# Optimization experiments

Measured on AMD Instinct MI355X. Metric: run time of the kernel, lower is better.

Reference implementation:

```python
import jax, jax.numpy as jnp
import numpy as np

N_NODES = 32768   # total atoms in the batch
N_EDGES = 65536   # directed bonds (avg degree ~2)
B = 512           # graphs per batch (graphs.batch_size)
D = 64            # in_feats = hidden_feats = 64
EH = 32           # edge-MLP hidden width
N_ITERS = 6       # num_step_set2set
N_LSTM = 3        # num_layer_set2set
EPS = 1e-5


def setup_inputs() -> dict:
    key = jax.random.key(0)
    ks = iter(jax.random.split(key, 64))
    nrm = lambda shape, s: jax.random.normal(next(ks), shape, dtype=jnp.float32) * s
    inp = {
        "atom_feats": jax.random.normal(next(ks), (N_NODES, D), dtype=jnp.float32),
        "edge_feat": jax.random.uniform(next(ks), (N_EDGES, 1), dtype=jnp.float32),
        "src": jax.random.randint(next(ks), (N_EDGES,), 0, N_NODES, dtype=jnp.int32),
        "dst": jax.random.randint(next(ks), (N_EDGES,), 0, N_NODES, dtype=jnp.int32),
        "node_graph_ids": jnp.sort(jax.random.randint(next(ks), (N_NODES,), 0, B, dtype=jnp.int32)),
    }
    for l in range(2):  # two NNConv layers
        inp[f"ew1_{l}"] = nrm((EH, 1), 0.5)
        inp[f"eb1_{l}"] = nrm((EH,), 0.1)
        inp[f"ew2_{l}"] = nrm((D * D, EH), 0.05)
        inp[f"eb2_{l}"] = nrm((D * D,), 0.02)
        inp[f"cb_{l}"] = nrm((D,), 0.1)
    inp["ln_g"] = jnp.ones((D,), jnp.float32)
    inp["ln_b"] = jnp.zeros((D,), jnp.float32)
    in_sizes = [2 * D, D, D]
    for l in range(N_LSTM):
        inp[f"wih{l}"] = nrm((4 * D, in_sizes[l]), 0.1)
        inp[f"whh{l}"] = nrm((4 * D, D), 0.1)
        inp[f"bih{l}"] = nrm((4 * D,), 0.05)
        inp[f"bhh{l}"] = nrm((4 * D,), 0.05)
    inp["gn_g"] = jnp.ones((2 * D,), jnp.float32)
    inp["gn_b"] = jnp.zeros((2 * D,), jnp.float32)
    inp["fc1_w"] = nrm((2 * D, 2 * D), 0.08)
    inp["fc1_b"] = nrm((2 * D,), 0.02)
    inp["bn_g"] = jnp.ones((2 * D,), jnp.float32)
    inp["bn_b"] = jnp.zeros((2 * D,), jnp.float32)
    inp["bn_m"] = jnp.zeros((2 * D,), jnp.float32)
    inp["bn_v"] = jnp.ones((2 * D,), jnp.float32)
    inp["fc2_w"] = nrm((D, 2 * D), 0.08)
    inp["fc2_b"] = nrm((D,), 0.02)
    return inp


def _layernorm(x, g, b):
    mu = jnp.mean(x, axis=-1, keepdims=True)
    v = jnp.var(x, axis=-1, keepdims=True)
    return (x - mu) / jnp.sqrt(v + EPS) * g + b


def _nnconv(x, edge_feat, src, dst, ew1, eb1, ew2, eb2, cb):
    # edge MLP: 1 -> 32 -> D*D, reshaped to a per-edge weight matrix
    h = jax.nn.relu(edge_feat @ ew1.T + eb1)              # [E, 32]
    W = (h @ ew2.T + eb2).reshape(-1, D, D)               # [E, D, D]
    m = jnp.einsum('ei,eio->eo', x[src], W)               # per-edge matmul [E, D]
    s = jax.ops.segment_sum(m, dst, num_segments=N_NODES)
    deg = jax.ops.segment_sum(jnp.ones((m.shape[0],), m.dtype), dst, num_segments=N_NODES)
    return s / jnp.maximum(deg, 1.0)[:, None] + cb        # scatter-mean + bias


def reference(atom_feats, edge_feat, src, dst, node_graph_ids,
              ew1_0, eb1_0, ew2_0, eb2_0, cb_0,
              ew1_1, eb1_1, ew2_1, eb2_1, cb_1,
              ln_g, ln_b,
              wih0, whh0, bih0, bhh0, wih1, whh1, bih1, bhh1, wih2, whh2, bih2, bhh2,
              gn_g, gn_b, fc1_w, fc1_b, bn_g, bn_b, bn_m, bn_v, fc2_w, fc2_b):
    x = atom_feats
    for (ew1, eb1, ew2, eb2, cb) in ((ew1_0, eb1_0, ew2_0, eb2_0, cb_0),
                                     (ew1_1, eb1_1, ew2_1, eb2_1, cb_1)):
        x = jax.nn.relu(_nnconv(x, edge_feat, src, dst, ew1, eb1, ew2, eb2, cb))
        # dropout is identity in eval mode
    x = _layernorm(x, ln_g, ln_b)  # graph_norm (num_nodes > batch_size)

    # Set2Set readout: 3-layer LSTM, 6 iterations, softmax attention per graph
    wihs = (wih0, wih1, wih2); whhs = (whh0, whh1, whh2)
    bihs = (bih0, bih1, bih2); bhhs = (bhh0, bhh1, bhh2)
    q_star = jnp.zeros((B, 2 * D), x.dtype)
    hs = [jnp.zeros((B, D), x.dtype) for _ in range(N_LSTM)]
    cs = [jnp.zeros((B, D), x.dtype) for _ in range(N_LSTM)]
    for _ in range(N_ITERS):
        inp_l = q_star
        for l in range(N_LSTM):
            gates = inp_l @ wihs[l].T + bihs[l] + hs[l] @ whhs[l].T + bhhs[l]
            ig, fg, gg, og = jnp.split(gates, 4, axis=-1)  # PyTorch gate order i,f,g,o
            cs[l] = jax.nn.sigmoid(fg) * cs[l] + jax.nn.sigmoid(ig) * jnp.tanh(gg)
            hs[l] = jax.nn.sigmoid(og) * jnp.tanh(cs[l])
            inp_l = hs[l]
        q = inp_l                                          # [B, D]
        e = jnp.sum(x * q[node_graph_ids], axis=-1)        # [N]
        mx = jax.ops.segment_max(e, node_graph_ids, num_segments=B)
        a = jnp.exp(e - mx[node_graph_ids])
        z = jax.ops.segment_sum(a, node_graph_ids, num_segments=B)
        alpha = a / z[node_graph_ids]                      # per-graph softmax
        readout = jax.ops.segment_sum(x * alpha[:, None], node_graph_ids, num_segments=B)
        q_star = jnp.concatenate([q, readout], axis=-1)    # [B, 2D]

    g = _layernorm(q_star, gn_g, gn_b)                     # GraphNorm on graph embedding
    y = g @ fc1_w.T + fc1_b
    y = (y - bn_m) / jnp.sqrt(bn_v + EPS) * bn_g + bn_b    # BatchNorm1d (eval, running stats)
    y = jax.nn.relu(y)
    out = jax.nn.relu(y @ fc2_w.T + fc2_b)                 # [B, D]
    return out
```

## Files before the change

kernel.cpp:

```cpp
#include <hip/hip_runtime.h>

#define KN 32768
#define KE 65536
#define KB 512
#define KEPB 64
#define KNREG 33
#define KEORD (KE + KNREG * KEPB)
#define KNBLK (KEORD / KEPB)

#define O_BUF0 ((size_t)0)
#define O_BUF1 (O_BUF0 + (size_t)KN * 64)
#define O_DEG  (O_BUF1 + (size_t)KN * 64)
#define O_GCNT (O_DEG + KN)
#define O_GST  (O_GCNT + KB)
#define O_HIST (O_GST + KB + 8)
#define O_CUR  (O_HIST + 128)
#define O_FLAG (O_CUR + 128)
#define O_ZEND (O_FLAG + 64)
#define O_EORD ((O_ZEND + 63) & ~(size_t)63)
#define O_RBLK (O_EORD + 2 * (size_t)KEORD)
#define O_FEND (O_RBLK + 2 * 1088)
#define O_WB   ((O_FEND + 63) & ~(size_t)63)
#define O_WS   (O_WB + (size_t)KNREG * 4096)
#define O_CROSS (O_WS + (size_t)KNREG * 4096)
#define O_RCNT (O_CROSS + 64)
#define O_AOFF (O_RCNT + 64)
#define O_REGN (O_AOFF + 128)
#define O_END  (O_REGN + KE)

#define T_WIH0 (O_EORD)
#define T_WHH0 (T_WIH0 + 32768)
#define T_WIH1 (T_WHH0 + 16384)
#define T_WHH1 (T_WIH1 + 16384)
#define T_WIH2 (T_WHH1 + 16384)
#define T_WHH2 (T_WIH2 + 16384)

__device__ float sigf(float x) { return 1.0f / (1.0f + expf(-x)); }

extern "C" __global__ void GNNModule_9259949490279_kernel(float* out, float v) {
    int i = blockIdx.x * 256 + threadIdx.x;
    if (i < KB * 64) out[i] = v;
}

extern "C" __global__ void k_post(const int* flag, float* out) {
    int f = flag[0];
    if (f == 0) return;
    int i = blockIdx.x * 256 + threadIdx.x;
    if (i < KB * 64) out[i] = 300.0f + (float)f;
}

extern "C" __global__ void k_init(float* wsf, int* wsi) {
    size_t i = (size_t)blockIdx.x * 256 + threadIdx.x;
    size_t stride = (size_t)gridDim.x * 256;
    for (size_t p = i; p < O_ZEND; p += stride) wsf[p] = 0.0f;
    for (size_t p = O_EORD + i; p < O_FEND; p += stride) wsi[p] = -1;
}

extern "C" __global__ void k_prepall(
    const float* ew1a, const float* eb1a, const float* ew1b, const float* eb1b,
    float* cross, int* rcnt) {
    __shared__ float la[32], lb_[32];
    int l = blockIdx.x;
    int t = threadIdx.x;
    const float* w = (l == 0) ? ew1a : ew1b;
    const float* b = (l == 0) ? eb1a : eb1b;
    if (t < 32) { la[t] = w[t]; lb_[t] = b[t]; }
    __syncthreads();
    if (t == 0) {
        float cl[32];
        int n = 0;
        for (int k = 0; k < 32; ++k) {
            float a = la[k], bb = lb_[k];
            if (a != 0.0f) {
                float tt = -bb / a;
                if (tt > 0.0f && tt < 1.0f) cl[n++] = tt;
            }
        }
        for (int i = 1; i < n; ++i) {
            float v = cl[i];
            int j = i - 1;
            while (j >= 0 && cl[j] > v) { cl[j + 1] = cl[j]; --j; }
            cl[j + 1] = v;
        }
        for (int i = 0; i < n; ++i) cross[32 * l + i] = cl[i];
        rcnt[l] = n;
    }
}

extern "C" __global__ void k_front(
    const int* dst, const int* gid, const float* efeat,
    const float* cross, const int* rcnt,
    float* deg, int* gcnt, int* hist0, int* hist1, int* flag) {
    __shared__ float c0[32], c1[32];
    __shared__ int n0s, n1s;
    __shared__ int lh0[64], lh1[64];
    __shared__ int lg[192];
    __shared__ int gminS;
    int t = threadIdx.x;
    int b = blockIdx.x;
    if (t < 32) { c0[t] = cross[t]; c1[t] = cross[32 + t]; }
    if (t == 0) { n0s = rcnt[0]; n1s = rcnt[1]; gminS = gid[b * 128]; }
    if (t < 64) { lh0[t] = 0; lh1[t] = 0; }
    if (t < 192) lg[t] = 0;
    __syncthreads();

    int e = b * 256 + t;
    int d = dst[e];
    if ((unsigned)d >= (unsigned)KN) { atomicOr(flag, 1); d = 0; }
    atomicAdd(&deg[d], 1.0f);
    float f = efeat[e];
    int r0 = 0, r1 = 0;
    int n0 = n0s, n1 = n1s;
    for (int j = 0; j < n0; ++j) r0 += (f > c0[j]) ? 1 : 0;
    for (int j = 0; j < n1; ++j) r1 += (f > c1[j]) ? 1 : 0;
    atomicAdd(&lh0[r0], 1);
    atomicAdd(&lh1[r1], 1);

    if (t < 128) {
        int n = b * 128 + t;
        int g = gid[n];
        if ((unsigned)g >= (unsigned)KB) { atomicOr(flag, 2); g = 0; }
        int gm = gminS;
        if ((unsigned)gm >= (unsigned)KB) gm = 0;
        int dd = g - gm;
        if (dd >= 0 && dd < 192) atomicAdd(&lg[dd], 1);
        else atomicAdd(&gcnt[g], 1);
    }
    __syncthreads();
    if (t < 64) {
        if (lh0[t] > 0) atomicAdd(&hist0[t], lh0[t]);
        if (lh1[t] > 0) atomicAdd(&hist1[t], lh1[t]);
    }
    if (t < 192 && lg[t] > 0) {
        int gm = gminS;
        if ((unsigned)gm >= (unsigned)KB) gm = 0;
        int gidx = gm + t;
        if (gidx <= KB) atomicAdd(&gcnt[gidx], lg[t]);
    }
}

extern "C" __global__ void k_scans(
    const int* gcnt, int* gstart,
    const int* histb, const int* rcnt, int* aoffb, int* rblkb) {
    int t = threadIdx.x;
    if (blockIdx.x == 0) {
        __shared__ int part[64];
        __shared__ int pre[64];
        int v[8];
        int s = 0;
        int base = t * 8;
        for (int j = 0; j < 8; ++j) { v[j] = gcnt[base + j]; s += v[j]; }
        part[t] = s;
        __syncthreads();
        if (t == 0) {
            int run = 0;
            for (int i = 0; i < 64; ++i) { pre[i] = run; run += part[i]; }
        }
        __syncthreads();
        int run = pre[t];
        for (int j = 0; j < 8; ++j) { gstart[base + j] = run; run += v[j]; }
        if (t == 63) gstart[KB] = run;
    } else {
        int l = blockIdx.x - 1;
        const int* hist = histb + l * 64;
        int* aoff = aoffb + l * 64;
        int* rblk = rblkb + l * 1088;
        __shared__ int lh[64];
        lh[t] = hist[t];
        __syncthreads();
        int R = rcnt[l] + 1;
        if (t < R) {
            int base = 0;
            for (int r = 0; r < t; ++r) base += (lh[r] + KEPB - 1) / KEPB;
            aoff[t] = base * KEPB;
            int nb = (lh[t] + KEPB - 1) / KEPB;
            for (int j = 0; j < nb; ++j) rblk[base + j] = t;
        }
    }
}

extern "C" __global__ __launch_bounds__(256) void k_mid(
    const float* efeat, const float* cross, const int* rcnt,
    const int* aoffb, int* cursorb, int* eorder0, int* eorder1,
    const float* ew1, const float* eb1, const float* ew2, const float* eb2,
    float* Wb, float* Ws) {
    int t = threadIdx.x;
    if (blockIdx.x < 256) {
        __shared__ float c0[32], c1[32];
        __shared__ int n0s, n1s;
        __shared__ int lc0[64], lc1[64], lb0[64], lb1[64];
        int b = blockIdx.x;
        if (t < 32) { c0[t] = cross[t]; c1[t] = cross[32 + t]; }
        if (t == 0) { n0s = rcnt[0]; n1s = rcnt[1]; }
        if (t < 64) { lc0[t] = 0; lc1[t] = 0; }
        __syncthreads();
        int e = b * 256 + t;
        float f = efeat[e];
        int r0 = 0, r1 = 0;
        int n0 = n0s, n1 = n1s;
        for (int j = 0; j < n0; ++j) r0 += (f > c0[j]) ? 1 : 0;
        for (int j = 0; j < n1; ++j) r1 += (f > c1[j]) ? 1 : 0;
        int lr0 = atomicAdd(&lc0[r0], 1);
        int lr1 = atomicAdd(&lc1[r1], 1);
        __syncthreads();
        if (t < 64) {
            if (lc0[t] > 0) lb0[t] = atomicAdd(&cursorb[t], lc0[t]);
            if (lc1[t] > 0) lb1[t] = atomicAdd(&cursorb[64 + t], lc1[t]);
        }
        __syncthreads();
        eorder0[aoffb[r0] + lb0[r0] + lr0] = e;
        eorder1[aoffb[64 + r1] + lb1[r1] + lr1] = e;
    } else {
        int r = blockIdx.x - 256;
        int n = rcnt[0];
        if (r > n) return;
        float lo = (r == 0) ? 0.0f : cross[r - 1];
        float hi = (r == n) ? 1.0f : cross[r];
        float mid = 0.5f * (lo + hi);
        __shared__ float mw[32], mb[32];
        if (t < 32) {
            bool act = (mid * ew1[t] + eb1[t]) > 0.0f;
            mw[t] = act ? ew1[t] : 0.0f;
            mb[t] = act ? eb1[t] : 0.0f;
        }
        __syncthreads();
        #pragma unroll
        for (int j = 0; j < 16; ++j) {
            int idx = j * 256 + t;
            float as = 0.0f, ab = eb2[idx];
            #pragma unroll
            for (int k4 = 0; k4 < 8; ++k4) {
                float4 w2 = *(const float4*)&ew2[(size_t)idx * 32 + 4 * k4];
                as += mw[4*k4+0]*w2.x + mw[4*k4+1]*w2.y + mw[4*k4+2]*w2.z + mw[4*k4+3]*w2.w;
                ab += mb[4*k4+0]*w2.x + mb[4*k4+1]*w2.y + mb[4*k4+2]*w2.z + mb[4*k4+3]*w2.w;
            }
            Wb[(size_t)r * 4096 + idx] = ab;
            Ws[(size_t)r * 4096 + idx] = as;
        }
    }
}

extern "C" __global__ __launch_bounds__(256) void k_mats(
    const float* ew1, const float* eb1, const float* ew2, const float* eb2,
    const float* cross, const int* rcnt, float* Wb, float* Ws) {
    int r = blockIdx.x;
    int n = *rcnt;
    if (r > n) return;
    float lo = (r == 0) ? 0.0f : cross[r - 1];
    float hi = (r == n) ? 1.0f : cross[r];
    float mid = 0.5f * (lo + hi);
    __shared__ float mw[32], mb[32];
    int t = threadIdx.x;
    if (t < 32) {
        bool act = (mid * ew1[t] + eb1[t]) > 0.0f;
        mw[t] = act ? ew1[t] : 0.0f;
        mb[t] = act ? eb1[t] : 0.0f;
    }
    __syncthreads();
    #pragma unroll
    for (int j = 0; j < 16; ++j) {
        int idx = j * 256 + t;
        float as = 0.0f, ab = eb2[idx];
        #pragma unroll
        for (int k4 = 0; k4 < 8; ++k4) {
            float4 w2 = *(const float4*)&ew2[(size_t)idx * 32 + 4 * k4];
            as += mw[4*k4+0]*w2.x + mw[4*k4+1]*w2.y + mw[4*k4+2]*w2.z + mw[4*k4+3]*w2.w;
            ab += mb[4*k4+0]*w2.x + mb[4*k4+1]*w2.y + mb[4*k4+2]*w2.z + mb[4*k4+3]*w2.w;
        }
        Wb[(size_t)r * 4096 + idx] = ab;
        Ws[(size_t)r * 4096 + idx] = as;
    }
}

extern "C" __global__ __launch_bounds__(256) void k_edge(
    const float* x, const float* efeat, const int* src, const int* dst,
    const float* Wb, const float* Ws, const int* rblk, const int* eorder,
    float* sbuf) {
    __shared__ __align__(16) float mbuf[4096];
    __shared__ __align__(16) float msuf[4096];
    __shared__ __align__(16) float xs[4][16][64];
    int b = blockIdx.x;
    int r = rblk[b];
    if (r < 0) return;
    int t = threadIdx.x;
    const float4* gb = (const float4*)(Wb + (size_t)r * 4096);
    const float4* gs = (const float4*)(Ws + (size_t)r * 4096);
    float4* lb = (float4*)mbuf;
    float4* ls = (float4*)msuf;
    #pragma unroll
    for (int j = 0; j < 4; ++j) {
        lb[t + 256 * j] = gb[t + 256 * j];
        ls[t + 256 * j] = gs[t + 256 * j];
    }
    __syncthreads();
    int w = t >> 6, lane = t & 63;
    int base = b * KEPB + w * 16;
    int eid = (lane < 16) ? eorder[base + lane] : -1;
    float efl = 0.0f;
    int srl = 0, dsl = 0;
    if (eid >= 0) { efl = efeat[eid]; srl = src[eid]; dsl = dst[eid]; }
    unsigned long long vm = __ballot(eid >= 0);
    if ((vm & 0xFFFFull) == 0ull) return;
    float ef[16];
    int dv[16];
    #pragma unroll
    for (int s = 0; s < 16; ++s) {
        ef[s] = __shfl(efl, s);
        int sv = __shfl(srl, s);
        dv[s] = __shfl(dsl, s);
        xs[w][s][lane] = x[(size_t)sv * 64 + lane];
    }
    float acc[16];
    #pragma unroll
    for (int s = 0; s < 16; ++s) acc[s] = 0.0f;
    #pragma unroll 1
    for (int i4 = 0; i4 < 16; ++i4) {
        float wb0 = mbuf[(i4 * 4 + 0) * 64 + lane], ws0 = msuf[(i4 * 4 + 0) * 64 + lane];
        float wb1 = mbuf[(i4 * 4 + 1) * 64 + lane], ws1 = msuf[(i4 * 4 + 1) * 64 + lane];
        float wb2 = mbuf[(i4 * 4 + 2) * 64 + lane], ws2 = msuf[(i4 * 4 + 2) * 64 + lane];
        float wb3 = mbuf[(i4 * 4 + 3) * 64 + lane], ws3 = msuf[(i4 * 4 + 3) * 64 + lane];
        #pragma unroll
        for (int j = 0; j < 16; ++j) {
            float4 xv = *(const float4*)&xs[w][j][i4 * 4];
            acc[j] = fmaf(xv.x, fmaf(ef[j], ws0, wb0), acc[j]);
            acc[j] = fmaf(xv.y, fmaf(ef[j], ws1, wb1), acc[j]);
            acc[j] = fmaf(xv.z, fmaf(ef[j], ws2, wb2), acc[j]);
            acc[j] = fmaf(xv.w, fmaf(ef[j], ws3, wb3), acc[j]);
        }
    }
    #pragma unroll
    for (int j = 0; j < 16; ++j) {
        if ((vm >> j) & 1ull) atomicAdd(&sbuf[(size_t)dv[j] * 64 + lane], acc[j]);
    }
}

extern "C" __global__ void k_final0(float* s, const float* deg, const float* cb, int* flag) {
    int idx = blockIdx.x * 256 + threadIdx.x;
    int n = idx >> 6;
    int o = idx & 63;
    float d = deg[n];
    if (d < 1.0f) d = 1.0f;
    float v = s[idx] / d + cb[o];
    if (v < 0.0f) v = 0.0f;
    if (!(v == v)) { v = 0.0f; atomicOr(flag, 32); }
    s[idx] = v;
}

extern "C" __global__ void k_final1ln(float* s, const float* deg, const float* cb,
                                      const float* lg, const float* lb, int* flag) {
    __shared__ float red[64];
    int t = threadIdx.x;
    int n = blockIdx.x;
    float d = deg[n];
    if (d < 1.0f) d = 1.0f;
    float v = s[(size_t)n * 64 + t] / d + cb[t];
    if (v < 0.0f) v = 0.0f;
    red[t] = v;
    __syncthreads();
    for (int m = 32; m >= 1; m >>= 1) {
        if (t < m) red[t] += red[t + m];
        __syncthreads();
    }
    float mu = red[0] * (1.0f / 64.0f);
    __syncthreads();
    red[t] = v * v;
    __syncthreads();
    for (int m = 32; m >= 1; m >>= 1) {
        if (t < m) red[t] += red[t + m];
        __syncthreads();
    }
    float var = red[0] * (1.0f / 64.0f) - mu * mu;
    float rs = rsqrtf(var + 1e-5f);
    float r = (v - mu) * rs * lg[t] + lb[t];
    if (!(r == r)) { r = 0.0f; atomicOr(flag, 8); }
    s[(size_t)n * 64 + t] = r;
}

extern "C" __global__ void k_twall(
    const float* wih0, const float* whh0, const float* wih1, const float* whh1,
    const float* wih2, const float* whh2, float4* dst) {
    int idx = blockIdx.x * 256 + threadIdx.x;
    if (idx >= 28672) return;
    const float* src;
    int K, local;
    if (idx < 8192)       { src = wih0; K = 128; local = idx; }
    else if (idx < 12288) { src = whh0; K = 64;  local = idx - 8192; }
    else if (idx < 16384) { src = wih1; K = 64;  local = idx - 12288; }
    else if (idx < 20480) { src = whh1; K = 64;  local = idx - 16384; }
    else if (idx < 24576) { src = wih2; K = 64;  local = idx - 20480; }
    else                  { src = whh2; K = 64;  local = idx - 24576; }
    int r = local & 255, k4 = local >> 8;
    const float* s = src + (size_t)r * K + 4 * k4;
    dst[idx] = make_float4(s[0], s[1], s[2], s[3]);
}

extern "C" __global__ __launch_bounds__(1024) void k_s2s9(
    const float* x, const int* gstart,
    const float4* wT0, const float4* uT0, const float* bih0, const float* bhh0,
    const float4* wT1, const float4* uT1, const float* bih1, const float* bhh1,
    const float4* wT2, const float4* uT2, const float* bih2, const float* bhh2,
    const float* gn_g, const float* gn_b,
    const float* fc1_w, const float* fc1_b,
    const float* bn_g, const float* bn_b, const float* bn_m, const float* bn_v,
    const float* fc2_w, const float* fc2_b,
    float* out, int* flag) {
    __shared__ __align__(16) float qs[128];
    __shared__ __align__(16) float hs0[64];
    __shared__ __align__(16) float hs1[64];
    __shared__ __align__(16) float hs2[64];
    __shared__ __align__(16) float cs[3][64];
    __shared__ __align__(16) float gatp[4][256];
    __shared__ __align__(16) float esc[1024];
    __shared__ __align__(16) float red16[16][64];
    __shared__ float mzz[16], zzz[16];
    int t = threadIdx.x;
    int g = blockIdx.x;
    int r = t & 255, q = t >> 8;
    int w = t >> 6, lane = t & 63;

    if (t < 128) qs[t] = 0.0f;
    if (t < 64) {
        hs0[t] = 0.0f; hs1[t] = 0.0f; hs2[t] = 0.0f;
        cs[0][t] = 0.0f; cs[1][t] = 0.0f; cs[2][t] = 0.0f;
    }
    __syncthreads();

    int n0 = gstart[g];
    int n1 = gstart[g + 1];
    if (n0 < 0) n0 = 0;
    if (n0 > KN) n0 = KN;
    if (n1 < n0) n1 = n0;
    if (n1 > KN) n1 = KN;
    int cnt = n1 - n0;
    if (cnt > 1024) { cnt = 1024; if (t == 0) atomicOr(flag, 16); }

    for (int it = 0; it < 6; ++it) {
        {
            float a = (q == 0) ? (bih0[r] + bhh0[r]) : 0.0f;
            const float4* wc = wT0 + (size_t)(q * 8) * 256 + r;
            const float4* q4 = (const float4*)qs + q * 8;
            #pragma unroll
            for (int k4 = 0; k4 < 8; ++k4) {
                float4 wv = wc[k4 * 256];
                float4 xv = q4[k4];
                a += wv.x*xv.x + wv.y*xv.y + wv.z*xv.z + wv.w*xv.w;
            }
            const float4* uc = uT0 + (size_t)(q * 4) * 256 + r;
            const float4* h4 = (const float4*)hs0 + q * 4;
            #pragma unroll
            for (int k4 = 0; k4 < 4; ++k4) {
                float4 wv = uc[k4 * 256];
                float4 hv = h4[k4];
                a += wv.x*hv.x + wv.y*hv.y + wv.z*hv.z + wv.w*hv.w;
            }
            gatp[q][r] = a;
            __syncthreads();
            if (t < 64) {
                float gi = gatp[0][t] + gatp[1][t] + gatp[2][t] + gatp[3][t];
                float gf = gatp[0][64 + t] + gatp[1][64 + t] + gatp[2][64 + t] + gatp[3][64 + t];
                float gg = gatp[0][128 + t] + gatp[1][128 + t] + gatp[2][128 + t] + gatp[3][128 + t];
                float go = gatp[0][192 + t] + gatp[1][192 + t] + gatp[2][192 + t] + gatp[3][192 + t];
                float c = sigf(gf) * cs[0][t] + sigf(gi) * tanhf(gg);
                cs[0][t] = c;
                hs0[t] = sigf(go) * tanhf(c);
            }
            __syncthreads();
        }
        {
            float a = (q == 0) ? (bih1[r] + bhh1[r]) : 0.0f;
            const float4* wc = wT1 + (size_t)(q * 4) * 256 + r;
            const float4* uc = uT1 + (size_t)(q * 4) * 256 + r;
            const float4* i4 = (const float4*)hs0 + q * 4;
            const float4* h4 = (const float4*)hs1 + q * 4;
            #pragma unroll
            for (int k4 = 0; k4 < 4; ++k4) {
                float4 wv = wc[k4 * 256];
                float4 xv = i4[k4];
                a += wv.x*xv.x + wv.y*xv.y + wv.z*xv.z + wv.w*xv.w;
                float4 uv = uc[k4 * 256];
                float4 hv = h4[k4];
                a += uv.x*hv.x + uv.y*hv.y + uv.z*hv.z + uv.w*hv.w;
            }
            gatp[q][r] = a;
            __syncthreads();
            if (t < 64) {
                float gi = gatp[0][t] + gatp[1][t] + gatp[2][t] + gatp[3][t];
                float gf = gatp[0][64 + t] + gatp[1][64 + t] + gatp[2][64 + t] + gatp[3][64 + t];
                float gg = gatp[0][128 + t] + gatp[1][128 + t] + gatp[2][128 + t] + gatp[3][128 + t];
                float go = gatp[0][192 + t] + gatp[1][192 + t] + gatp[2][192 + t] + gatp[3][192 + t];
                float c = sigf(gf) * cs[1][t] + sigf(gi) * tanhf(gg);
                cs[1][t] = c;
                hs1[t] = sigf(go) * tanhf(c);
            }
            __syncthreads();
        }
        {
            float a = (q == 0) ? (bih2[r] + bhh2[r]) : 0.0f;
            const float4* wc = wT2 + (size_t)(q * 4) * 256 + r;
            const float4* uc = uT2 + (size_t)(q * 4) * 256 + r;
            const float4* i4 = (const float4*)hs1 + q * 4;
            const float4* h4 = (const float4*)hs2 + q * 4;
            #pragma unroll
            for (int k4 = 0; k4 < 4; ++k4) {
                float4 wv = wc[k4 * 256];
                float4 xv = i4[k4];
                a += wv.x*xv.x + wv.y*xv.y + wv.z*xv.z + wv.w*xv.w;
                float4 uv = uc[k4 * 256];
                float4 hv = h4[k4];
                a += uv.x*hv.x + uv.y*hv.y + uv.z*hv.z + uv.w*hv.w;
            }
            gatp[q][r] = a;
            __syncthreads();
            if (t < 64) {
                float gi = gatp[0][t] + gatp[1][t] + gatp[2][t] + gatp[3][t];
                float gf = gatp[0][64 + t] + gatp[1][64 + t] + gatp[2][64 + t] + gatp[3][64 + t];
                float gg = gatp[0][128 + t] + gatp[1][128 + t] + gatp[2][128 + t] + gatp[3][128 + t];
                float go = gatp[0][192 + t] + gatp[1][192 + t] + gatp[2][192 + t] + gatp[3][192 + t];
                float c = sigf(gf) * cs[2][t] + sigf(gi) * tanhf(gg);
                cs[2][t] = c;
                hs2[t] = sigf(go) * tanhf(c);
            }
            __syncthreads();
        }
        {
            float qv_ = hs2[lane];
            float mx = -3.0e38f;
            for (int p = w; p < cnt; p += 16) {
                float xv = x[(size_t)(n0 + p) * 64 + lane];
                float v = xv * qv_;
                v += __shfl_xor(v, 1);
                v += __shfl_xor(v, 2);
                v += __shfl_xor(v, 4);
                v += __shfl_xor(v, 8);
                v += __shfl_xor(v, 16);
                v += __shfl_xor(v, 32);
                if (lane == 0) esc[p] = v;
                if (v > mx) mx = v;
            }
            if (lane == 0) mzz[w] = mx;
            __syncthreads();
            float M = mzz[0];
            #pragma unroll
            for (int j = 1; j < 16; ++j) if (mzz[j] > M) M = mzz[j];
            float z = 0.0f;
            for (int p = t; p < cnt; p += 1024) {
                float e = expf(esc[p] - M);
                esc[p] = e;
                z += e;
            }
            z += __shfl_xor(z, 1);
            z += __shfl_xor(z, 2);
            z += __shfl_xor(z, 4);
            z += __shfl_xor(z, 8);
            z += __shfl_xor(z, 16);
            z += __shfl_xor(z, 32);
            if (lane == 0) zzz[w] = z;
            __syncthreads();
            float Z = 0.0f;
            #pragma unroll
            for (int j = 0; j < 16; ++j) Z += zzz[j];
            float rd = 0.0f;
            for (int p = w; p < cnt; p += 16)
                rd += x[(size_t)(n0 + p) * 64 + lane] * esc[p];
            red16[w][lane] = rd;
            __syncthreads();
            if (t < 64) {
                float rr = 0.0f;
                #pragma unroll
                for (int j = 0; j < 16; ++j) rr += red16[j][t];
                rr = (cnt > 0 && Z > 0.0f) ? rr / Z : 0.0f;
                qs[t] = hs2[t];
                qs[64 + t] = rr;
            }
            __syncthreads();
        }
    }

    {
        float v = (t < 128) ? qs[t] : 0.0f;
        float s1 = v, s2 = v * v;
        s1 += __shfl_xor(s1, 1); s2 += __shfl_xor(s2, 1);
        s1 += __shfl_xor(s1, 2); s2 += __shfl_xor(s2, 2);
        s1 += __shfl_xor(s1, 4); s2 += __shfl_xor(s2, 4);
        s1 += __shfl_xor(s1, 8); s2 += __shfl_xor(s2, 8);
        s1 += __shfl_xor(s1, 16); s2 += __shfl_xor(s2, 16);
        s1 += __shfl_xor(s1, 32); s2 += __shfl_xor(s2, 32);
        if (lane == 0) { mzz[w] = s1; zzz[w] = s2; }
        __syncthreads();
        float sm = mzz[0] + mzz[1];
        float sq = zzz[0] + zzz[1];
        float mu = sm * (1.0f / 128.0f);
        float var = sq * (1.0f / 128.0f) - mu * mu;
        float rs = rsqrtf(var + 1e-5f);
        if (t < 128) esc[t] = (v - mu) * rs * gn_g[t] + gn_b[t];
        __syncthreads();
        if (t < 128) {
            float y = fc1_b[t];
            const float4* wr = (const float4*)(fc1_w + (size_t)t * 128);
            #pragma unroll
            for (int k4 = 0; k4 < 32; ++k4) {
                float4 wv = wr[k4];
                float4 gv = *(const float4*)&esc[4 * k4];
                y += wv.x*gv.x + wv.y*gv.y + wv.z*gv.z + wv.w*gv.w;
            }
            y = (y - bn_m[t]) * rsqrtf(bn_v[t] + 1e-5f) * bn_g[t] + bn_b[t];
            if (y < 0.0f) y = 0.0f;
            gatp[0][t] = y;
        }
        __syncthreads();
        if (t < 64) {
            float o = fc2_b[t];
            const float4* wr = (const float4*)(fc2_w + (size_t)t * 128);
            #pragma unroll
            for (int k4 = 0; k4 < 32; ++k4) {
                float4 wv = wr[k4];
                float4 yv = *(const float4*)&gatp[0][4 * k4];
                o += wv.x*yv.x + wv.y*yv.y + wv.z*yv.z + wv.w*yv.w;
            }
            if (!(o == o)) o = 999.0f;
            else if (o < 0.0f) o = 0.0f;
            out[(size_t)g * 64 + t] = o;
        }
    }
}

extern "C" void kernel_launch(void* const* d_in, const int* in_sizes, int n_in,
                              void* d_out, int out_size, void* d_ws, size_t ws_size,
                              hipStream_t stream) {
    float* out = (float*)d_out;
    const int outBlocks = (KB * 64 + 255) / 256;

    if (n_in != 39) {
        GNNModule_9259949490279_kernel<<<outBlocks, 256, 0, stream>>>(out, 50.0f);
        return;
    }
    if (in_sizes[0] != KN * 64 || in_sizes[1] != KE || in_sizes[4] != KN) {
        GNNModule_9259949490279_kernel<<<outBlocks, 256, 0, stream>>>(out, 60.0f);
        return;
    }
    if (out_size != KB * 64) {
        GNNModule_9259949490279_kernel<<<outBlocks, 256, 0, stream>>>(out, 80.0f);
        return;
    }
    if (ws_size < O_END * 4) {
        GNNModule_9259949490279_kernel<<<outBlocks, 256, 0, stream>>>(out, 100.0f);
        return;
    }

    const float* atom = (const float*)d_in[0];
    const float* efeat = (const float*)d_in[1];
    const int* src = (const int*)d_in[2];
    const int* dst = (const int*)d_in[3];
    const int* gid = (const int*)d_in[4];
    const float* ew1[2] = {(const float*)d_in[5], (const float*)d_in[10]};
    const float* eb1[2] = {(const float*)d_in[6], (const float*)d_in[11]};
    const float* ew2[2] = {(const float*)d_in[7], (const float*)d_in[12]};
    const float* eb2[2] = {(const float*)d_in[8], (const float*)d_in[13]};
    const float* cb[2] = {(const float*)d_in[9], (const float*)d_in[14]};
    const float* ln_g = (const float*)d_in[15];
    const float* ln_b = (const float*)d_in[16];
    const float* wih0 = (const float*)d_in[17];
    const float* whh0 = (const float*)d_in[18];
    const float* bih0 = (const float*)d_in[19];
    const float* bhh0 = (const float*)d_in[20];
    const float* wih1 = (const float*)d_in[21];
    const float* whh1 = (const float*)d_in[22];
    const float* bih1 = (const float*)d_in[23];
    const float* bhh1 = (const float*)d_in[24];
    const float* wih2 = (const float*)d_in[25];
    const float* whh2 = (const float*)d_in[26];
    const float* bih2 = (const float*)d_in[27];
    const float* bhh2 = (const float*)d_in[28];
    const float* gn_g = (const float*)d_in[29];
    const float* gn_b = (const float*)d_in[30];
    const float* fc1_w = (const float*)d_in[31];
    const float* fc1_b = (const float*)d_in[32];
    const float* bn_g = (const float*)d_in[33];
    const float* bn_b = (const float*)d_in[34];
    const float* bn_m = (const float*)d_in[35];
    const float* bn_v = (const float*)d_in[36];
    const float* fc2_w = (const float*)d_in[37];
    const float* fc2_b = (const float*)d_in[38];

    float* wsf = (float*)d_ws;
    int* wsi = (int*)d_ws;
    float* buf0 = wsf + O_BUF0;
    float* buf1 = wsf + O_BUF1;
    float* deg = wsf + O_DEG;
    int* gcnt = wsi + O_GCNT;
    int* gstart = wsi + O_GST;
    int* flag = wsi + O_FLAG;
    float* Wb = wsf + O_WB;
    float* Ws = wsf + O_WS;
    float* cross = wsf + O_CROSS;
    int* rcnt = wsi + O_RCNT;

    k_init<<<2048, 256, 0, stream>>>(wsf, wsi);

    k_prepall<<<2, 64, 0, stream>>>(ew1[0], eb1[0], ew1[1], eb1[1], cross, rcnt);

    k_front<<<256, 256, 0, stream>>>(dst, gid, efeat, cross, rcnt,
                                     deg, gcnt, wsi + O_HIST, wsi + O_HIST + 64, flag);

    k_scans<<<3, 64, 0, stream>>>(gcnt, gstart, wsi + O_HIST, rcnt,
                                  wsi + O_AOFF, wsi + O_RBLK);

    k_mid<<<289, 256, 0, stream>>>(efeat, cross, rcnt, wsi + O_AOFF, wsi + O_CUR,
                                   wsi + O_EORD, wsi + O_EORD + KEORD,
                                   ew1[0], eb1[0], ew2[0], eb2[0], Wb, Ws);

    k_edge<<<KNBLK, 256, 0, stream>>>(atom, efeat, src, dst, Wb, Ws,
                                      wsi + O_RBLK, wsi + O_EORD, buf0);
    k_final0<<<KN * 64 / 256, 256, 0, stream>>>(buf0, deg, cb[0], flag);

    k_mats<<<KNREG, 256, 0, stream>>>(ew1[1], eb1[1], ew2[1], eb2[1],
                                      cross + 32, rcnt + 1, Wb, Ws);
    k_edge<<<KNBLK, 256, 0, stream>>>(buf0, efeat, src, dst, Wb, Ws,
                                      wsi + O_RBLK + 1088, wsi + O_EORD + KEORD, buf1);
    k_final1ln<<<KN, 64, 0, stream>>>(buf1, deg, cb[1], ln_g, ln_b, flag);

    float4* twbase = (float4*)(wsf + T_WIH0);
    k_twall<<<112, 256, 0, stream>>>(wih0, whh0, wih1, whh1, wih2, whh2, twbase);

    k_s2s9<<<KB, 1024, 0, stream>>>(buf1, gstart,
        twbase, (float4*)(wsf + T_WHH0), bih0, bhh0,
        (float4*)(wsf + T_WIH1), (float4*)(wsf + T_WHH1), bih1, bhh1,
        (float4*)(wsf + T_WIH2), (float4*)(wsf + T_WHH2), bih2, bhh2,
        gn_g, gn_b, fc1_w, fc1_b, bn_g, bn_b, bn_m, bn_v, fc2_w, fc2_b,
        out, flag);

    k_post<<<outBlocks, 256, 0, stream>>>(flag, out);
}
```

Before: 335.3 us.

## Merge finalize kernels with weight prep and fuse softmax-readout passes

Merges the layer-0 finalize with the layer-1 edge-matrix build, and the layer-1 finalize/LayerNorm with the LSTM weight transpose, into single launches that branch on block index. This removes two launches. The LayerNorm now uses wavefront shuffles with four nodes per 256-thread block instead of a shared-memory tree reduction over 64-thread blocks. In the set2set attention, the exp pass and the weighted readout pass become one loop that accumulates Z and the readout together, dropping a barrier and the scratch write of the exp values. The unused region buffer is removed from the workspace layout.

```diff
diff --git a/kernel.cpp b/kernel.cpp
--- a/kernel.cpp
+++ b/kernel.cpp
@@ -25,8 +25,7 @@
 #define O_CROSS (O_WS + (size_t)KNREG * 4096)
 #define O_RCNT (O_CROSS + 64)
 #define O_AOFF (O_RCNT + 64)
-#define O_REGN (O_AOFF + 128)
-#define O_END  (O_REGN + KE)
+#define O_END  (O_AOFF + 128)
 
 #define T_WIH0 (O_EORD)
 #define T_WHH0 (T_WIH0 + 32768)
@@ -103,7 +102,6 @@
     if (t < 64) { lh0[t] = 0; lh1[t] = 0; }
     if (t < 192) lg[t] = 0;
     __syncthreads();
-
     int e = b * 256 + t;
     int d = dst[e];
     if ((unsigned)d >= (unsigned)KN) { atomicOr(flag, 1); d = 0; }
@@ -115,7 +113,6 @@
     for (int j = 0; j < n1; ++j) r1 += (f > c1[j]) ? 1 : 0;
     atomicAdd(&lh0[r0], 1);
     atomicAdd(&lh1[r1], 1);
-
     if (t < 128) {
         int n = b * 128 + t;
         int g = gid[n];
@@ -237,38 +234,6 @@
             Wb[(size_t)r * 4096 + idx] = ab;
             Ws[(size_t)r * 4096 + idx] = as;
         }
-    }
-}
-
-extern "C" __global__ __launch_bounds__(256) void k_mats(
-    const float* ew1, const float* eb1, const float* ew2, const float* eb2,
-    const float* cross, const int* rcnt, float* Wb, float* Ws) {
-    int r = blockIdx.x;
-    int n = *rcnt;
-    if (r > n) return;
-    float lo = (r == 0) ? 0.0f : cross[r - 1];
-    float hi = (r == n) ? 1.0f : cross[r];
-    float mid = 0.5f * (lo + hi);
-    __shared__ float mw[32], mb[32];
-    int t = threadIdx.x;
-    if (t < 32) {
-        bool act = (mid * ew1[t] + eb1[t]) > 0.0f;
-        mw[t] = act ? ew1[t] : 0.0f;
-        mb[t] = act ? eb1[t] : 0.0f;
-    }
-    __syncthreads();
-    #pragma unroll
-    for (int j = 0; j < 16; ++j) {
-        int idx = j * 256 + t;
-        float as = 0.0f, ab = eb2[idx];
-        #pragma unroll
-        for (int k4 = 0; k4 < 8; ++k4) {
-            float4 w2 = *(const float4*)&ew2[(size_t)idx * 32 + 4 * k4];
-            as += mw[4*k4+0]*w2.x + mw[4*k4+1]*w2.y + mw[4*k4+2]*w2.z + mw[4*k4+3]*w2.w;
-            ab += mb[4*k4+0]*w2.x + mb[4*k4+1]*w2.y + mb[4*k4+2]*w2.z + mb[4*k4+3]*w2.w;
-        }
-        Wb[(size_t)r * 4096 + idx] = ab;
-        Ws[(size_t)r * 4096 + idx] = as;
     }
 }
 
@@ -334,67 +299,95 @@
     }
 }
 
-extern "C" __global__ void k_final0(float* s, const float* deg, const float* cb, int* flag) {
-    int idx = blockIdx.x * 256 + threadIdx.x;
-    int n = idx >> 6;
-    int o = idx & 63;
-    float d = deg[n];
-    if (d < 1.0f) d = 1.0f;
-    float v = s[idx] / d + cb[o];
-    if (v < 0.0f) v = 0.0f;
-    if (!(v == v)) { v = 0.0f; atomicOr(flag, 32); }
-    s[idx] = v;
-}
-
-extern "C" __global__ void k_final1ln(float* s, const float* deg, const float* cb,
-                                      const float* lg, const float* lb, int* flag) {
-    __shared__ float red[64];
+extern "C" __global__ __launch_bounds__(256) void k_fin0mats(
+    float* s, const float* deg, const float* cb, int* flag,
+    const float* ew1, const float* eb1, const float* ew2, const float* eb2,
+    const float* cross, const int* rcnt, float* Wb, float* Ws) {
     int t = threadIdx.x;
-    int n = blockIdx.x;
-    float d = deg[n];
-    if (d < 1.0f) d = 1.0f;
-    float v = s[(size_t)n * 64 + t] / d + cb[t];
-    if (v < 0.0f) v = 0.0f;
-    red[t] = v;
-    __syncthreads();
-    for (int m = 32; m >= 1; m >>= 1) {
-        if (t < m) red[t] += red[t + m];
-        __syncthreads();
-    }
-    float mu = red[0] * (1.0f / 64.0f);
-    __syncthreads();
-    red[t] = v * v;
-    __syncthreads();
-    for (int m = 32; m >= 1; m >>= 1) {
-        if (t < m) red[t] += red[t + m];
-        __syncthreads();
-    }
-    float var = red[0] * (1.0f / 64.0f) - mu * mu;
-    float rs = rsqrtf(var + 1e-5f);
-    float r = (v - mu) * rs * lg[t] + lb[t];
-    if (!(r == r)) { r = 0.0f; atomicOr(flag, 8); }
-    s[(size_t)n * 64 + t] = r;
-}
-
-extern "C" __global__ void k_twall(
+    if (blockIdx.x < 8192) {
+        int idx = blockIdx.x * 256 + t;
+        int n = idx >> 6;
+        int o = idx & 63;
+        float d = deg[n];
+        if (d < 1.0f) d = 1.0f;
+        float v = s[idx] / d + cb[o];
+        if (v < 0.0f) v = 0.0f;
+        if (!(v == v)) { v = 0.0f; atomicOr(flag, 32); }
+        s[idx] = v;
+    } else {
+        int r = blockIdx.x - 8192;
+        int n = *rcnt;
+        if (r > n) return;
+        float lo = (r == 0) ? 0.0f : cross[r - 1];
+        float hi = (r == n) ? 1.0f : cross[r];
+        float mid = 0.5f * (lo + hi);
+        __shared__ float mw[32], mb[32];
+        if (t < 32) {
+            bool act = (mid * ew1[t] + eb1[t]) > 0.0f;
+            mw[t] = act ? ew1[t] : 0.0f;
+            mb[t] = act ? eb1[t] : 0.0f;
+        }
+        __syncthreads();
+        #pragma unroll
+        for (int j = 0; j < 16; ++j) {
+            int idx = j * 256 + t;
+            float as = 0.0f, ab = eb2[idx];
+            #pragma unroll
+            for (int k4 = 0; k4 < 8; ++k4) {
+                float4 w2 = *(const float4*)&ew2[(size_t)idx * 32 + 4 * k4];
+                as += mw[4*k4+0]*w2.x + mw[4*k4+1]*w2.y + mw[4*k4+2]*w2.z + mw[4*k4+3]*w2.w;
+                ab += mb[4*k4+0]*w2.x + mb[4*k4+1]*w2.y + mb[4*k4+2]*w2.z + mb[4*k4+3]*w2.w;
+            }
+            Wb[(size_t)r * 4096 + idx] = ab;
+            Ws[(size_t)r * 4096 + idx] = as;
+        }
+    }
+}
+
+extern "C" __global__ __launch_bounds__(256) void k_fin1tw(
+    float* s, const float* deg, const float* cb,
+    const float* lg, const float* lb, int* flag,
     const float* wih0, const float* whh0, const float* wih1, const float* whh1,
     const float* wih2, const float* whh2, float4* dst) {
-    int idx = blockIdx.x * 256 + threadIdx.x;
-    if (idx >= 28672) return;
-    const float* src;
-    int K, local;
-    if (idx < 8192)       { src = wih0; K = 128; local = idx; }
-    else if (idx < 12288) { src = whh0; K = 64;  local = idx - 8192; }
-    else if (idx < 16384) { src = wih1; K = 64;  local = idx - 12288; }
-    else if (idx < 20480) { src = whh1; K = 64;  local = idx - 16384; }
-    else if (idx < 24576) { src = wih2; K = 64;  local = idx - 20480; }
-    else                  { src = whh2; K = 64;  local = idx - 24576; }
-    int r = local & 255, k4 = local >> 8;
-    const float* s = src + (size_t)r * K + 4 * k4;
-    dst[idx] = make_float4(s[0], s[1], s[2], s[3]);
-}
-
-extern "C" __global__ __launch_bounds__(1024) void k_s2s9(
+    int t = threadIdx.x;
+    if (blockIdx.x < 8192) {
+        int w = t >> 6, lane = t & 63;
+        int n = blockIdx.x * 4 + w;
+        float d = deg[n];
+        if (d < 1.0f) d = 1.0f;
+        float v = s[(size_t)n * 64 + lane] / d + cb[lane];
+        if (v < 0.0f) v = 0.0f;
+        float sm = v, sq = v * v;
+        sm += __shfl_xor(sm, 1); sq += __shfl_xor(sq, 1);
+        sm += __shfl_xor(sm, 2); sq += __shfl_xor(sq, 2);
+        sm += __shfl_xor(sm, 4); sq += __shfl_xor(sq, 4);
+        sm += __shfl_xor(sm, 8); sq += __shfl_xor(sq, 8);
+        sm += __shfl_xor(sm, 16); sq += __shfl_xor(sq, 16);
+        sm += __shfl_xor(sm, 32); sq += __shfl_xor(sq, 32);
+        float mu = sm * (1.0f / 64.0f);
+        float var = sq * (1.0f / 64.0f) - mu * mu;
+        float rs = rsqrtf(var + 1e-5f);
+        float r = (v - mu) * rs * lg[lane] + lb[lane];
+        if (!(r == r)) { r = 0.0f; atomicOr(flag, 8); }
+        s[(size_t)n * 64 + lane] = r;
+    } else {
+        int idx = (blockIdx.x - 8192) * 256 + t;
+        if (idx >= 28672) return;
+        const float* src;
+        int K, local;
+        if (idx < 8192)       { src = wih0; K = 128; local = idx; }
+        else if (idx < 12288) { src = whh0; K = 64;  local = idx - 8192; }
+        else if (idx < 16384) { src = wih1; K = 64;  local = idx - 12288; }
+        else if (idx < 20480) { src = whh1; K = 64;  local = idx - 16384; }
+        else if (idx < 24576) { src = wih2; K = 64;  local = idx - 20480; }
+        else                  { src = whh2; K = 64;  local = idx - 24576; }
+        int r = local & 255, k4 = local >> 8;
+        const float* sp = src + (size_t)r * K + 4 * k4;
+        dst[idx] = make_float4(sp[0], sp[1], sp[2], sp[3]);
+    }
+}
+
+extern "C" __global__ __launch_bounds__(1024) void k_s2s10(
     const float* x, const int* gstart,
     const float4* wT0, const float4* uT0, const float* bih0, const float* bhh0,
     const float4* wT1, const float4* uT1, const float* bih1, const float* bhh1,
@@ -542,29 +535,20 @@
             float M = mzz[0];
             #pragma unroll
             for (int j = 1; j < 16; ++j) if (mzz[j] > M) M = mzz[j];
-            float z = 0.0f;
-            for (int p = t; p < cnt; p += 1024) {
+            float z = 0.0f, rd = 0.0f;
+            for (int p = w; p < cnt; p += 16) {
                 float e = expf(esc[p] - M);
-                esc[p] = e;
+                float xv = x[(size_t)(n0 + p) * 64 + lane];
                 z += e;
-            }
-            z += __shfl_xor(z, 1);
-            z += __shfl_xor(z, 2);
-            z += __shfl_xor(z, 4);
-            z += __shfl_xor(z, 8);
-            z += __shfl_xor(z, 16);
-            z += __shfl_xor(z, 32);
+                rd += e * xv;
+            }
             if (lane == 0) zzz[w] = z;
-            __syncthreads();
-            float Z = 0.0f;
-            #pragma unroll
-            for (int j = 0; j < 16; ++j) Z += zzz[j];
-            float rd = 0.0f;
-            for (int p = w; p < cnt; p += 16)
-                rd += x[(size_t)(n0 + p) * 64 + lane] * esc[p];
             red16[w][lane] = rd;
             __syncthreads();
             if (t < 64) {
+                float Z = 0.0f;
+                #pragma unroll
+                for (int j = 0; j < 16; ++j) Z += zzz[j];
                 float rr = 0.0f;
                 #pragma unroll
                 for (int j = 0; j < 16; ++j) rr += red16[j][t];
@@ -642,7 +626,7 @@
         GNNModule_9259949490279_kernel<<<outBlocks, 256, 0, stream>>>(out, 80.0f);
         return;
     }
-    if (ws_size < O_END * 4) {
+    if (ws_size < (O_END > O_WS + (size_t)KNREG * 4096 ? O_END : O_WS + (size_t)KNREG * 4096) * 4) {
         GNNModule_9259949490279_kernel<<<outBlocks, 256, 0, stream>>>(out, 100.0f);
         return;
     }
@@ -711,18 +695,18 @@
 
     k_edge<<<KNBLK, 256, 0, stream>>>(atom, efeat, src, dst, Wb, Ws,
                                       wsi + O_RBLK, wsi + O_EORD, buf0);
-    k_final0<<<KN * 64 / 256, 256, 0, stream>>>(buf0, deg, cb[0], flag);
-
-    k_mats<<<KNREG, 256, 0, stream>>>(ew1[1], eb1[1], ew2[1], eb2[1],
-                                      cross + 32, rcnt + 1, Wb, Ws);
+
+    k_fin0mats<<<8192 + KNREG, 256, 0, stream>>>(buf0, deg, cb[0], flag,
+        ew1[1], eb1[1], ew2[1], eb2[1], cross + 32, rcnt + 1, Wb, Ws);
+
     k_edge<<<KNBLK, 256, 0, stream>>>(buf0, efeat, src, dst, Wb, Ws,
                                       wsi + O_RBLK + 1088, wsi + O_EORD + KEORD, buf1);
-    k_final1ln<<<KN, 64, 0, stream>>>(buf1, deg, cb[1], ln_g, ln_b, flag);
 
     float4* twbase = (float4*)(wsf + T_WIH0);
-    k_twall<<<112, 256, 0, stream>>>(wih0, whh0, wih1, whh1, wih2, whh2, twbase);
-
-    k_s2s9<<<KB, 1024, 0, stream>>>(buf1, gstart,
+    k_fin1tw<<<8192 + 112, 256, 0, stream>>>(buf1, deg, cb[1], ln_g, ln_b, flag,
+        wih0, whh0, wih1, whh1, wih2, whh2, twbase);
+
+    k_s2s10<<<KB, 1024, 0, stream>>>(buf1, gstart,
         twbase, (float4*)(wsf + T_WHH0), bih0, bhh0,
         (float4*)(wsf + T_WIH1), (float4*)(wsf + T_WHH1), bih1, bhh1,
         (float4*)(wsf + T_WIH2), (float4*)(wsf + T_WHH2), bih2, bhh2,
```

New measurement: 332.1 us, median of 2. About the same (-0.9%).
